# Kernel optimization log

Hardware: AMD Instinct MI355X
Metric: run time of the kernel (lower is better)

The kernel has to match this reference:

```python
import jax, jax.numpy as jnp
import numpy as np

B, M, D, DP = 8192, 64, 128, 128

def setup_inputs() -> dict:
    key = jax.random.key(0)
    kx, kq, kk, kv, kr = jax.random.split(key, 5)
    scale = 1.0 / np.sqrt(D)  # keep softmax logits in a sane range
    return {
        "x": jax.random.normal(kx, (B, M, D), dtype=jnp.float32),
        "Wq": jax.random.normal(kq, (D, DP), dtype=jnp.float32) * scale,
        "Wk": jax.random.normal(kk, (D, DP), dtype=jnp.float32) * scale,
        "Wv": jax.random.normal(kv, (D, DP), dtype=jnp.float32) * scale,
        "Wr": jax.random.normal(kr, (D, DP), dtype=jnp.float32) * scale,
    }

def reference(x, Wq, Wk, Wv, Wr):
    # Shared per-field linear projections (Product layer): [B, M, d] @ [d, d'] -> [B, M, d']
    q = jnp.einsum('bmd,de->bme', x, Wq)
    k = jnp.einsum('bmd,de->bme', x, Wk)
    v = jnp.einsum('bmd,de->bme', x, Wv)
    r = jnp.einsum('bmd,de->bme', x, Wr)
    # Field-wise attention: scores [B, M, M], softmax over last axis (axis=2)
    scores = jnp.einsum('bme,bne->bmn', q, k)
    alphas = jax.nn.softmax(scores, axis=2)
    new_e = jnp.einsum('bmn,bne->bme', alphas, v)
    return jax.nn.relu(r + new_e)
```

## Files before the change

kernel.cpp:

```cpp
#include <hip/hip_runtime.h>

typedef _Float16 half8 __attribute__((ext_vector_type(8)));
typedef _Float16 half4 __attribute__((ext_vector_type(4)));
typedef float floatx4 __attribute__((ext_vector_type(4)));

#define NB 8
#define SX 136
#define SVT 72
#define SP 80

__global__ void wconv_kernel(const float* __restrict__ Wq, const float* __restrict__ Wk,
                             const float* __restrict__ Wv, const float* __restrict__ Wr,
                             _Float16* __restrict__ Wh) {
    int idx = blockIdx.x * 256 + threadIdx.x;
    int row = idx >> 9;
    int col = idx & 511;
    const float* s = (col < 128) ? Wq : (col < 256) ? Wk : (col < 384) ? Wv : Wr;
    Wh[idx] = (_Float16)s[row * 128 + (col & 127)];
}

__global__ __launch_bounds__(512, 2)
void autoint_kernel(const float* __restrict__ xg, const _Float16* __restrict__ Wh,
                    float* __restrict__ outg) {
    const int tid  = threadIdx.x;
    const int w    = tid >> 6;
    const int lane = tid & 63;
    const int nn   = lane & 15;
    const int q    = lane >> 4;
    const long b0  = (long)blockIdx.x * NB;

    __shared__ _Float16 lds[31744];
    _Float16* Xs = lds;
    _Float16* Vt = lds;
    _Float16* Qs = lds + 9216;
    _Float16* Ks = lds + 17920;
    _Float16* Ps = lds + 26624;

    half8 wf[4][4];
    #pragma unroll
    for (int c = 0; c < 4; ++c) {
        int ctg;
        if (w < 4) ctg = 4 * w + c;
        else       ctg = (c < 2) ? (16 + 2 * (w - 4) + c) : (24 + 2 * (w - 4) + (c - 2));
        int col = ctg * 16 + nn;
        #pragma unroll
        for (int ks = 0; ks < 4; ++ks) {
            half8 f;
            #pragma unroll
            for (int i = 0; i < 8; ++i)
                f[i] = Wh[(ks * 32 + q * 8 + i) * 512 + col];
            wf[c][ks] = f;
        }
    }

    float4 pf[8];
    if (w < 4) {
        const float4* Xg = (const float4*)(xg + b0 * 8192);
        #pragma unroll
        for (int t = 0; t < 8; ++t) pf[t] = Xg[t * 256 + tid];
        #pragma unroll
        for (int t = 0; t < 8; ++t) {
            int g = t * 256 + tid;
            int row = g >> 5, c4 = (g & 31) * 4;
            half4 h = { (_Float16)pf[t].x, (_Float16)pf[t].y,
                        (_Float16)pf[t].z, (_Float16)pf[t].w };
            *(half4*)(Xs + row * SX + c4) = h;
        }
    }
    __syncthreads();

    for (int it = 0; it < NB; ++it) {
        const long b = b0 + it;

        if (w < 4 && it + 1 < NB) {
            const float4* Xg = (const float4*)(xg + (b + 1) * 8192);
            #pragma unroll
            for (int t = 0; t < 8; ++t) pf[t] = Xg[t * 256 + tid];
        }

        floatx4 acc[4][4];
        {
            floatx4 z = {0.f, 0.f, 0.f, 0.f};
            #pragma unroll
            for (int rt = 0; rt < 4; ++rt)
                #pragma unroll
                for (int c = 0; c < 4; ++c) acc[rt][c] = z;
        }
        #pragma unroll
        for (int ks = 0; ks < 4; ++ks) {
            half8 a[4];
            #pragma unroll
            for (int rt = 0; rt < 4; ++rt)
                a[rt] = *(const half8*)(Xs + (rt * 16 + nn) * SX + ks * 32 + q * 8);
            #pragma unroll
            for (int rt = 0; rt < 4; ++rt)
                #pragma unroll
                for (int c = 0; c < 4; ++c)
                    acc[rt][c] = __builtin_amdgcn_mfma_f32_16x16x32_f16(
                        a[rt], wf[c][ks], acc[rt][c], 0, 0, 0);
        }
        __syncthreads();

        if (w < 2) {
            #pragma unroll
            for (int rt = 0; rt < 4; ++rt)
                #pragma unroll
                for (int c = 0; c < 4; ++c) {
                    int f = (4 * w + c) * 16 + nn;
                    #pragma unroll
                    for (int r = 0; r < 4; ++r)
                        Qs[(rt * 16 + q * 4 + r) * SX + f] = (_Float16)acc[rt][c][r];
                }
        } else if (w < 4) {
            #pragma unroll
            for (int rt = 0; rt < 4; ++rt)
                #pragma unroll
                for (int c = 0; c < 4; ++c) {
                    int f = (4 * w + c - 8) * 16 + nn;
                    #pragma unroll
                    for (int r = 0; r < 4; ++r)
                        Ks[(rt * 16 + q * 4 + r) * SX + f] = (_Float16)acc[rt][c][r];
                }
        } else {
            int j = w - 4;
            #pragma unroll
            for (int rt = 0; rt < 4; ++rt)
                #pragma unroll
                for (int c = 0; c < 2; ++c) {
                    int f = (2 * j + c) * 16 + nn;
                    half4 hv = { (_Float16)acc[rt][c][0], (_Float16)acc[rt][c][1],
                                 (_Float16)acc[rt][c][2], (_Float16)acc[rt][c][3] };
                    *(half4*)(Vt + f * SVT + rt * 16 + q * 4) = hv;
                }
        }
        __syncthreads();

        if (w < 4) {
            floatx4 sacc[4];
            {
                floatx4 z = {0.f, 0.f, 0.f, 0.f};
                #pragma unroll
                for (int c = 0; c < 4; ++c) sacc[c] = z;
            }
            #pragma unroll
            for (int ks = 0; ks < 4; ++ks) {
                half8 aq = *(const half8*)(Qs + (w * 16 + nn) * SX + ks * 32 + q * 8);
                #pragma unroll
                for (int c = 0; c < 4; ++c) {
                    half8 bk = *(const half8*)(Ks + (c * 16 + nn) * SX + ks * 32 + q * 8);
                    sacc[c] = __builtin_amdgcn_mfma_f32_16x16x32_f16(aq, bk, sacc[c], 0, 0, 0);
                }
            }
            #pragma unroll
            for (int r = 0; r < 4; ++r) {
                float mx = fmaxf(fmaxf(sacc[0][r], sacc[1][r]), fmaxf(sacc[2][r], sacc[3][r]));
                mx = fmaxf(mx, __shfl_xor(mx, 1));
                mx = fmaxf(mx, __shfl_xor(mx, 2));
                mx = fmaxf(mx, __shfl_xor(mx, 4));
                mx = fmaxf(mx, __shfl_xor(mx, 8));
                float e0 = __expf(sacc[0][r] - mx);
                float e1 = __expf(sacc[1][r] - mx);
                float e2 = __expf(sacc[2][r] - mx);
                float e3 = __expf(sacc[3][r] - mx);
                float s = e0 + e1 + e2 + e3;
                s += __shfl_xor(s, 1);
                s += __shfl_xor(s, 2);
                s += __shfl_xor(s, 4);
                s += __shfl_xor(s, 8);
                float inv = 1.0f / s;
                int row = w * 16 + q * 4 + r;
                Ps[row * SP + 0 * 16 + nn] = (_Float16)(e0 * inv);
                Ps[row * SP + 1 * 16 + nn] = (_Float16)(e1 * inv);
                Ps[row * SP + 2 * 16 + nn] = (_Float16)(e2 * inv);
                Ps[row * SP + 3 * 16 + nn] = (_Float16)(e3 * inv);
            }
        }
        __syncthreads();

        if (w >= 4) {
            int j = w - 4;
            floatx4 pv[4][2];
            {
                floatx4 z = {0.f, 0.f, 0.f, 0.f};
                #pragma unroll
                for (int rt = 0; rt < 4; ++rt) { pv[rt][0] = z; pv[rt][1] = z; }
            }
            #pragma unroll
            for (int ks = 0; ks < 2; ++ks) {
                half8 ap[4];
                #pragma unroll
                for (int rt = 0; rt < 4; ++rt)
                    ap[rt] = *(const half8*)(Ps + (rt * 16 + nn) * SP + ks * 32 + q * 8);
                #pragma unroll
                for (int cl = 0; cl < 2; ++cl) {
                    half8 bv = *(const half8*)(Vt + ((2 * j + cl) * 16 + nn) * SVT + ks * 32 + q * 8);
                    #pragma unroll
                    for (int rt = 0; rt < 4; ++rt)
                        pv[rt][cl] = __builtin_amdgcn_mfma_f32_16x16x32_f16(ap[rt], bv, pv[rt][cl], 0, 0, 0);
                }
            }
            float* ob = outg + b * 8192;
            #pragma unroll
            for (int rt = 0; rt < 4; ++rt)
                #pragma unroll
                for (int cl = 0; cl < 2; ++cl) {
                    int colb = (2 * j + cl) * 16 + nn;
                    #pragma unroll
                    for (int r = 0; r < 4; ++r) {
                        int row = rt * 16 + q * 4 + r;
                        float v = acc[rt][2 + cl][r] + pv[rt][cl][r];
                        ob[row * 128 + colb] = fmaxf(v, 0.0f);
                    }
                }
        }
        __syncthreads();

        if (w < 4 && it + 1 < NB) {
            #pragma unroll
            for (int t = 0; t < 8; ++t) {
                int g = t * 256 + tid;
                int row = g >> 5, c4 = (g & 31) * 4;
                half4 h = { (_Float16)pf[t].x, (_Float16)pf[t].y,
                            (_Float16)pf[t].z, (_Float16)pf[t].w };
                *(half4*)(Xs + row * SX + c4) = h;
            }
        }
        __syncthreads();
    }
}

extern "C" void kernel_launch(void* const* d_in, const int* in_sizes, int n_in,
                              void* d_out, int out_size, void* d_ws, size_t ws_size,
                              hipStream_t stream) {
    const float* x  = (const float*)d_in[0];
    const float* Wq = (const float*)d_in[1];
    const float* Wk = (const float*)d_in[2];
    const float* Wv = (const float*)d_in[3];
    const float* Wr = (const float*)d_in[4];
    _Float16* Wh = (_Float16*)d_ws;
    float* out = (float*)d_out;

    wconv_kernel<<<256, 256, 0, stream>>>(Wq, Wk, Wv, Wr, Wh);
    autoint_kernel<<<1024, 512, 0, stream>>>(x, Wh, out);
}
```

Measured before the change: 477.7 us.

## Fold Wq·Wkᵀ into one weight so scores become (xG)xᵀ, rebalance waves

Precomputes G = Wq·Wkᵀ in the weight-prep kernel, so the kernel projects x through only three weight sets (G, Wv, Wr) and computes scores as (xG)·xᵀ instead of forming Q and K separately. All eight waves now share every stage evenly. The weights are pre-swizzled into MFMA fragment order for vectorized loads, and the batch per block and LDS footprint are reduced to raise occupancy and launch twice as many blocks. This removes a quarter of the projection MFMAs and one LDS stage, but rounding G to fp16 changes numerical error, and the tighter launch bound may cause register pressure.

```diff
diff --git a/kernel.cpp b/kernel.cpp
--- a/kernel.cpp
+++ b/kernel.cpp
@@ -4,63 +4,70 @@
 typedef _Float16 half4 __attribute__((ext_vector_type(4)));
 typedef float floatx4 __attribute__((ext_vector_type(4)));
 
-#define NB 8
+#define NB 4
 #define SX 136
 #define SVT 72
-#define SP 80
-
-__global__ void wconv_kernel(const float* __restrict__ Wq, const float* __restrict__ Wk,
+#define SP 72
+
+__global__ void wprep_kernel(const float* __restrict__ Wq, const float* __restrict__ Wk,
                              const float* __restrict__ Wv, const float* __restrict__ Wr,
-                             _Float16* __restrict__ Wh) {
-    int idx = blockIdx.x * 256 + threadIdx.x;
-    int row = idx >> 9;
-    int col = idx & 511;
-    const float* s = (col < 128) ? Wq : (col < 256) ? Wk : (col < 384) ? Wv : Wr;
-    Wh[idx] = (_Float16)s[row * 128 + (col & 127)];
+                             _Float16* __restrict__ W2) {
+    int idx  = blockIdx.x * 256 + threadIdx.x;
+    int i    = idx & 7;
+    int lane = (idx >> 3) & 63;
+    int ks   = (idx >> 9) & 3;
+    int ctg  = idx >> 11;
+    int q = lane >> 4, nn = lane & 15;
+    int k = ks * 32 + q * 8 + i;
+    float v;
+    if (ctg < 8) {
+        int e = ctg * 16 + nn;
+        float s = 0.f;
+        #pragma unroll 8
+        for (int c = 0; c < 128; ++c) s += Wq[k * 128 + c] * Wk[e * 128 + c];
+        v = s;
+    } else if (ctg < 16) {
+        v = Wv[k * 128 + (ctg - 8) * 16 + nn];
+    } else {
+        v = Wr[k * 128 + (ctg - 16) * 16 + nn];
+    }
+    W2[idx] = (_Float16)v;
 }
 
-__global__ __launch_bounds__(512, 2)
-void autoint_kernel(const float* __restrict__ xg, const _Float16* __restrict__ Wh,
+__global__ __launch_bounds__(512, 6)
+void autoint_kernel(const float* __restrict__ xg, const _Float16* __restrict__ W2,
                     float* __restrict__ outg) {
     const int tid  = threadIdx.x;
     const int w    = tid >> 6;
     const int lane = tid & 63;
     const int nn   = lane & 15;
     const int q    = lane >> 4;
+    const int rb   = w & 3;
     const long b0  = (long)blockIdx.x * NB;
 
-    __shared__ _Float16 lds[31744];
+    __shared__ _Float16 lds[26624];
     _Float16* Xs = lds;
-    _Float16* Vt = lds;
-    _Float16* Qs = lds + 9216;
-    _Float16* Ks = lds + 17920;
-    _Float16* Ps = lds + 26624;
-
-    half8 wf[4][4];
+    _Float16* Gs = lds + 8704;
+    _Float16* Ps = Gs;
+    _Float16* Vt = lds + 17408;
+
+    half8 wf[3][4];
     #pragma unroll
-    for (int c = 0; c < 4; ++c) {
-        int ctg;
-        if (w < 4) ctg = 4 * w + c;
-        else       ctg = (c < 2) ? (16 + 2 * (w - 4) + c) : (24 + 2 * (w - 4) + (c - 2));
-        int col = ctg * 16 + nn;
-        #pragma unroll
-        for (int ks = 0; ks < 4; ++ks) {
-            half8 f;
-            #pragma unroll
-            for (int i = 0; i < 8; ++i)
-                f[i] = Wh[(ks * 32 + q * 8 + i) * 512 + col];
-            wf[c][ks] = f;
-        }
-    }
-
-    float4 pf[8];
-    if (w < 4) {
+    for (int c = 0; c < 3; ++c) {
+        int ctg = c * 8 + w;
+        #pragma unroll
+        for (int ks = 0; ks < 4; ++ks)
+            wf[c][ks] = *(const half8*)(W2 + ((ctg * 4 + ks) * 64 + lane) * 8);
+    }
+
+    float4 pf[4];
+    {
         const float4* Xg = (const float4*)(xg + b0 * 8192);
         #pragma unroll
-        for (int t = 0; t < 8; ++t) pf[t] = Xg[t * 256 + tid];
-        #pragma unroll
-        for (int t = 0; t < 8; ++t) {
-            int g = t * 256 + tid;
+        for (int t = 0; t < 4; ++t) pf[t] = Xg[t * 512 + tid];
+        #pragma unroll
+        for (int t = 0; t < 4; ++t) {
+            int g = t * 512 + tid;
             int row = g >> 5, c4 = (g & 31) * 4;
             half4 h = { (_Float16)pf[t].x, (_Float16)pf[t].y,
                         (_Float16)pf[t].z, (_Float16)pf[t].w };
@@ -72,19 +79,19 @@
     for (int it = 0; it < NB; ++it) {
         const long b = b0 + it;
 
-        if (w < 4 && it + 1 < NB) {
+        if (it + 1 < NB) {
             const float4* Xg = (const float4*)(xg + (b + 1) * 8192);
             #pragma unroll
-            for (int t = 0; t < 8; ++t) pf[t] = Xg[t * 256 + tid];
-        }
-
-        floatx4 acc[4][4];
+            for (int t = 0; t < 4; ++t) pf[t] = Xg[t * 512 + tid];
+        }
+
+        floatx4 acc[4][3];
         {
             floatx4 z = {0.f, 0.f, 0.f, 0.f};
             #pragma unroll
             for (int rt = 0; rt < 4; ++rt)
                 #pragma unroll
-                for (int c = 0; c < 4; ++c) acc[rt][c] = z;
+                for (int c = 0; c < 3; ++c) acc[rt][c] = z;
         }
         #pragma unroll
         for (int ks = 0; ks < 4; ++ks) {
@@ -95,136 +102,102 @@
             #pragma unroll
             for (int rt = 0; rt < 4; ++rt)
                 #pragma unroll
-                for (int c = 0; c < 4; ++c)
+                for (int c = 0; c < 3; ++c)
                     acc[rt][c] = __builtin_amdgcn_mfma_f32_16x16x32_f16(
                         a[rt], wf[c][ks], acc[rt][c], 0, 0, 0);
         }
-        __syncthreads();
-
-        if (w < 2) {
-            #pragma unroll
-            for (int rt = 0; rt < 4; ++rt)
-                #pragma unroll
-                for (int c = 0; c < 4; ++c) {
-                    int f = (4 * w + c) * 16 + nn;
-                    #pragma unroll
-                    for (int r = 0; r < 4; ++r)
-                        Qs[(rt * 16 + q * 4 + r) * SX + f] = (_Float16)acc[rt][c][r];
-                }
-        } else if (w < 4) {
-            #pragma unroll
-            for (int rt = 0; rt < 4; ++rt)
-                #pragma unroll
-                for (int c = 0; c < 4; ++c) {
-                    int f = (4 * w + c - 8) * 16 + nn;
-                    #pragma unroll
-                    for (int r = 0; r < 4; ++r)
-                        Ks[(rt * 16 + q * 4 + r) * SX + f] = (_Float16)acc[rt][c][r];
-                }
-        } else {
-            int j = w - 4;
-            #pragma unroll
-            for (int rt = 0; rt < 4; ++rt)
-                #pragma unroll
-                for (int c = 0; c < 2; ++c) {
-                    int f = (2 * j + c) * 16 + nn;
-                    half4 hv = { (_Float16)acc[rt][c][0], (_Float16)acc[rt][c][1],
-                                 (_Float16)acc[rt][c][2], (_Float16)acc[rt][c][3] };
-                    *(half4*)(Vt + f * SVT + rt * 16 + q * 4) = hv;
-                }
-        }
-        __syncthreads();
-
-        if (w < 4) {
-            floatx4 sacc[4];
-            {
-                floatx4 z = {0.f, 0.f, 0.f, 0.f};
-                #pragma unroll
-                for (int c = 0; c < 4; ++c) sacc[c] = z;
-            }
-            #pragma unroll
-            for (int ks = 0; ks < 4; ++ks) {
-                half8 aq = *(const half8*)(Qs + (w * 16 + nn) * SX + ks * 32 + q * 8);
-                #pragma unroll
-                for (int c = 0; c < 4; ++c) {
-                    half8 bk = *(const half8*)(Ks + (c * 16 + nn) * SX + ks * 32 + q * 8);
-                    sacc[c] = __builtin_amdgcn_mfma_f32_16x16x32_f16(aq, bk, sacc[c], 0, 0, 0);
-                }
-            }
-            #pragma unroll
-            for (int r = 0; r < 4; ++r) {
-                float mx = fmaxf(fmaxf(sacc[0][r], sacc[1][r]), fmaxf(sacc[2][r], sacc[3][r]));
-                mx = fmaxf(mx, __shfl_xor(mx, 1));
-                mx = fmaxf(mx, __shfl_xor(mx, 2));
-                mx = fmaxf(mx, __shfl_xor(mx, 4));
-                mx = fmaxf(mx, __shfl_xor(mx, 8));
-                float e0 = __expf(sacc[0][r] - mx);
-                float e1 = __expf(sacc[1][r] - mx);
-                float e2 = __expf(sacc[2][r] - mx);
-                float e3 = __expf(sacc[3][r] - mx);
-                float s = e0 + e1 + e2 + e3;
-                s += __shfl_xor(s, 1);
-                s += __shfl_xor(s, 2);
-                s += __shfl_xor(s, 4);
-                s += __shfl_xor(s, 8);
-                float inv = 1.0f / s;
-                int row = w * 16 + q * 4 + r;
-                Ps[row * SP + 0 * 16 + nn] = (_Float16)(e0 * inv);
-                Ps[row * SP + 1 * 16 + nn] = (_Float16)(e1 * inv);
-                Ps[row * SP + 2 * 16 + nn] = (_Float16)(e2 * inv);
-                Ps[row * SP + 3 * 16 + nn] = (_Float16)(e3 * inv);
-            }
-        }
-        __syncthreads();
-
-        if (w >= 4) {
-            int j = w - 4;
-            floatx4 pv[4][2];
-            {
-                floatx4 z = {0.f, 0.f, 0.f, 0.f};
-                #pragma unroll
-                for (int rt = 0; rt < 4; ++rt) { pv[rt][0] = z; pv[rt][1] = z; }
-            }
-            #pragma unroll
-            for (int ks = 0; ks < 2; ++ks) {
-                half8 ap[4];
-                #pragma unroll
-                for (int rt = 0; rt < 4; ++rt)
-                    ap[rt] = *(const half8*)(Ps + (rt * 16 + nn) * SP + ks * 32 + q * 8);
-                #pragma unroll
-                for (int cl = 0; cl < 2; ++cl) {
-                    half8 bv = *(const half8*)(Vt + ((2 * j + cl) * 16 + nn) * SVT + ks * 32 + q * 8);
-                    #pragma unroll
-                    for (int rt = 0; rt < 4; ++rt)
-                        pv[rt][cl] = __builtin_amdgcn_mfma_f32_16x16x32_f16(ap[rt], bv, pv[rt][cl], 0, 0, 0);
-                }
-            }
-            float* ob = outg + b * 8192;
-            #pragma unroll
-            for (int rt = 0; rt < 4; ++rt)
-                #pragma unroll
-                for (int cl = 0; cl < 2; ++cl) {
-                    int colb = (2 * j + cl) * 16 + nn;
-                    #pragma unroll
-                    for (int r = 0; r < 4; ++r) {
-                        int row = rt * 16 + q * 4 + r;
-                        float v = acc[rt][2 + cl][r] + pv[rt][cl][r];
-                        ob[row * 128 + colb] = fmaxf(v, 0.0f);
-                    }
-                }
-        }
-        __syncthreads();
-
-        if (w < 4 && it + 1 < NB) {
-            #pragma unroll
-            for (int t = 0; t < 8; ++t) {
-                int g = t * 256 + tid;
+        #pragma unroll
+        for (int rt = 0; rt < 4; ++rt) {
+            #pragma unroll
+            for (int r = 0; r < 4; ++r)
+                Gs[(rt * 16 + q * 4 + r) * SX + w * 16 + nn] = (_Float16)acc[rt][0][r];
+            half4 hv = { (_Float16)acc[rt][1][0], (_Float16)acc[rt][1][1],
+                         (_Float16)acc[rt][1][2], (_Float16)acc[rt][1][3] };
+            *(half4*)(Vt + (w * 16 + nn) * SVT + rt * 16 + q * 4) = hv;
+        }
+        __syncthreads();
+
+        floatx4 sacc[4];
+        {
+            floatx4 z = {0.f, 0.f, 0.f, 0.f};
+            #pragma unroll
+            for (int ct = 0; ct < 4; ++ct) sacc[ct] = z;
+        }
+        #pragma unroll
+        for (int ks = 0; ks < 4; ++ks) {
+            half8 ag = *(const half8*)(Gs + (rb * 16 + nn) * SX + ks * 32 + q * 8);
+            #pragma unroll
+            for (int ct = 0; ct < 4; ++ct) {
+                half8 bx = *(const half8*)(Xs + (ct * 16 + nn) * SX + ks * 32 + q * 8);
+                sacc[ct] = __builtin_amdgcn_mfma_f32_16x16x32_f16(ag, bx, sacc[ct], 0, 0, 0);
+            }
+        }
+        float pvals[4][2];
+        const int ct0 = (w >> 2) * 2;
+        #pragma unroll
+        for (int r = 0; r < 4; ++r) {
+            float mx = fmaxf(fmaxf(sacc[0][r], sacc[1][r]), fmaxf(sacc[2][r], sacc[3][r]));
+            mx = fmaxf(mx, __shfl_xor(mx, 1));
+            mx = fmaxf(mx, __shfl_xor(mx, 2));
+            mx = fmaxf(mx, __shfl_xor(mx, 4));
+            mx = fmaxf(mx, __shfl_xor(mx, 8));
+            float e0 = __expf(sacc[0][r] - mx);
+            float e1 = __expf(sacc[1][r] - mx);
+            float e2 = __expf(sacc[2][r] - mx);
+            float e3 = __expf(sacc[3][r] - mx);
+            float s = e0 + e1 + e2 + e3;
+            s += __shfl_xor(s, 1);
+            s += __shfl_xor(s, 2);
+            s += __shfl_xor(s, 4);
+            s += __shfl_xor(s, 8);
+            float inv = 1.0f / s;
+            pvals[r][0] = ((ct0 == 0) ? e0 : e2) * inv;
+            pvals[r][1] = ((ct0 == 0) ? e1 : e3) * inv;
+        }
+        __syncthreads();
+
+        #pragma unroll
+        for (int r = 0; r < 4; ++r) {
+            int row = rb * 16 + q * 4 + r;
+            Ps[row * SP + (ct0 + 0) * 16 + nn] = (_Float16)pvals[r][0];
+            Ps[row * SP + (ct0 + 1) * 16 + nn] = (_Float16)pvals[r][1];
+        }
+        if (it + 1 < NB) {
+            #pragma unroll
+            for (int t = 0; t < 4; ++t) {
+                int g = t * 512 + tid;
                 int row = g >> 5, c4 = (g & 31) * 4;
                 half4 h = { (_Float16)pf[t].x, (_Float16)pf[t].y,
                             (_Float16)pf[t].z, (_Float16)pf[t].w };
                 *(half4*)(Xs + row * SX + c4) = h;
             }
         }
+        __syncthreads();
+
+        floatx4 pv[4];
+        {
+            floatx4 z = {0.f, 0.f, 0.f, 0.f};
+            #pragma unroll
+            for (int rt = 0; rt < 4; ++rt) pv[rt] = z;
+        }
+        #pragma unroll
+        for (int ks = 0; ks < 2; ++ks) {
+            half8 bv = *(const half8*)(Vt + (w * 16 + nn) * SVT + ks * 32 + q * 8);
+            #pragma unroll
+            for (int rt = 0; rt < 4; ++rt) {
+                half8 ap = *(const half8*)(Ps + (rt * 16 + nn) * SP + ks * 32 + q * 8);
+                pv[rt] = __builtin_amdgcn_mfma_f32_16x16x32_f16(ap, bv, pv[rt], 0, 0, 0);
+            }
+        }
+        float* ob = outg + b * 8192;
+        #pragma unroll
+        for (int rt = 0; rt < 4; ++rt)
+            #pragma unroll
+            for (int r = 0; r < 4; ++r) {
+                int row = rt * 16 + q * 4 + r;
+                float v = acc[rt][2][r] + pv[rt][r];
+                ob[row * 128 + w * 16 + nn] = fmaxf(v, 0.0f);
+            }
         __syncthreads();
     }
 }
@@ -237,9 +210,9 @@
     const float* Wk = (const float*)d_in[2];
     const float* Wv = (const float*)d_in[3];
     const float* Wr = (const float*)d_in[4];
-    _Float16* Wh = (_Float16*)d_ws;
+    _Float16* W2 = (_Float16*)d_ws;
     float* out = (float*)d_out;
 
-    wconv_kernel<<<256, 256, 0, stream>>>(Wq, Wk, Wv, Wr, Wh);
-    autoint_kernel<<<1024, 512, 0, stream>>>(x, Wh, out);
+    wprep_kernel<<<192, 256, 0, stream>>>(Wq, Wk, Wv, Wr, W2);
+    autoint_kernel<<<2048, 512, 0, stream>>>(x, W2, out);
 }
```

Result: slower. 941.9 us (+97.2%).
